# Kernel tuning notes

Hardware: AMD Instinct MI355X
Metric: run time of the kernel (lower is better)

## Reference

```python
import jax, jax.numpy as jnp
import numpy as np

D_MODEL = 1024
N_HEADS = 16
D_K = D_MODEL // N_HEADS  # 64
SCALE = 1.0 / np.sqrt(D_K).astype(np.float32)


def setup_inputs() -> dict:
    key = jax.random.key(0)
    kx, kq, kk, kv, ko = jax.random.split(key, 5)
    B, S = 2, 2048
    s = 0.02  # keep pre-softmax logits in a sane range
    return {
        "x": jax.random.normal(kx, (B, S, D_MODEL), dtype=jnp.float32),
        "Wq": jax.random.normal(kq, (D_MODEL, D_MODEL), dtype=jnp.float32) * s,
        "Wk": jax.random.normal(kk, (D_MODEL, D_MODEL), dtype=jnp.float32) * s,
        "Wv": jax.random.normal(kv, (D_MODEL, D_MODEL), dtype=jnp.float32) * s,
        "Wo": jax.random.normal(ko, (D_MODEL, D_MODEL), dtype=jnp.float32) * s,
    }


def reference(x, Wq, Wk, Wv, Wo):
    # x: [B, S, D]; nn.Linear(bias=False) computes x @ W.T
    B, S, D = x.shape
    H, dk = N_HEADS, D_K

    def proj(W):
        # [B, S, D] -> [B, H, S, dk]
        return (x @ W.T).reshape(B, S, H, dk).transpose(0, 2, 1, 3)

    q = proj(Wq)
    k = proj(Wk)
    v = proj(Wv)

    # Flash tiling with online softmax is exact full attention (no mask):
    scores = jnp.einsum("bhqd,bhkd->bhqk", q, k) * SCALE  # [B,H,S,S]
    p = jax.nn.softmax(scores, axis=-1)
    o = jnp.einsum("bhqk,bhkd->bhqd", p, v)               # [B,H,S,dk]

    o = o.transpose(0, 2, 1, 3).reshape(B, S, D)
    return o @ Wo.T
```

## Files before the change

kernel.cpp:

```cpp
#include <hip/hip_runtime.h>
#include <cstdint>

typedef __attribute__((ext_vector_type(8))) __bf16 bf16x8;
typedef __attribute__((ext_vector_type(4))) float f32x4;
using u16 = unsigned short;
using u32 = unsigned int;

#define D_MODEL 1024
#define N_HEADS 16
#define D_K     64
#define SEQ     2048
#define BATCH   2
#define NTOKENS (BATCH * SEQ)
#define SCALE   0.125f
#define LOG2E   1.44269504088896340736f
#define C2      (SCALE * LOG2E)

__device__ __forceinline__ u16 f32_to_bf16(float f) {
    union { float f; u32 u; } v; v.f = f;
    u32 r = (v.u + 0x7fffu + ((v.u >> 16) & 1u)) >> 16;
    return (u16)r;
}

__device__ __forceinline__ u32 cvt_pk_bf16(float a, float b) {
    u32 r;
    asm("v_cvt_pk_bf16_f32 %0, %1, %2" : "=v"(r) : "v"(a), "v"(b));
    return r;
}

typedef const __attribute__((address_space(1))) u32* gas_ptr;
typedef __attribute__((address_space(3))) u32* las_ptr;
__device__ __forceinline__ void gl2lds16(const u16* g, u16* l) {
    __builtin_amdgcn_global_load_lds((gas_ptr)g, (las_ptr)l, 16, 0, 0);
}

__global__ __launch_bounds__(256) void cvt_all(const float* __restrict__ x,
                                               const float* __restrict__ Wq, const float* __restrict__ Wk,
                                               const float* __restrict__ Wv, const float* __restrict__ Wo,
                                               u16* __restrict__ xb,
                                               u16* __restrict__ wq, u16* __restrict__ wk,
                                               u16* __restrict__ wv, u16* __restrict__ wo) {
    const int NX = NTOKENS * D_MODEL;
    size_t i = (size_t)(blockIdx.x * 256 + threadIdx.x) * 4;
    const float* src; u16* dst; size_t off;
    if (i < (size_t)NX) { src = x; dst = xb; off = i; }
    else {
        size_t j = i - NX;
        int w = (int)(j >> 20);
        off = j & ((1u << 20) - 1);
        src = (w == 0) ? Wq : (w == 1) ? Wk : (w == 2) ? Wv : Wo;
        dst = (w == 0) ? wq : (w == 1) ? wk : (w == 2) ? wv : wo;
    }
    float4 f = *(const float4*)(src + off);
    u32 lo = (u32)f32_to_bf16(f.x) | ((u32)f32_to_bf16(f.y) << 16);
    u32 hi = (u32)f32_to_bf16(f.z) | ((u32)f32_to_bf16(f.w) << 16);
    uint2 o; o.x = lo; o.y = hi;
    size_t osw = (off & ~(size_t)63) | ((((off >> 3) & 7) ^ ((off >> 10) & 7)) << 3) | (off & 7);
    *(uint2*)(dst + osw) = o;
}

__device__ __forceinline__ void gemm_core_128(const u16* __restrict__ Ab,
                                              const u16* __restrict__ Bb,
                                              u16* __restrict__ sm,
                                              f32x4 acc[4][4]) {
    const int tid  = threadIdx.x;
    const int wave = tid >> 6, lane = tid & 63;
    const int quad = lane >> 4, l4 = lane & 15, s7 = l4 & 7;
    const int wm = wave >> 1, wn = wave & 1;

    const int srow = tid >> 3, sch = tid & 7;
    const u16* Asrc = Ab + (size_t)srow * D_MODEL + sch * 8;
    const u16* Bsrc = Bb + (size_t)srow * D_MODEL + sch * 8;

#define STG8(base_, kt_) do {                                                         \
    const size_t ko_ = (size_t)(kt_) * 64;                                            \
    u16* const Ad_ = sm + (base_) + wave * 512;                                       \
    u16* const Bd_ = sm + (base_) + 8192 + wave * 512;                                \
    _Pragma("unroll")                                                                 \
    for (int c_ = 0; c_ < 4; c_++)                                                    \
        gl2lds16(Asrc + (size_t)c_ * 32 * D_MODEL + ko_, Ad_ + c_ * 2048);            \
    _Pragma("unroll")                                                                 \
    for (int c_ = 0; c_ < 4; c_++)                                                    \
        gl2lds16(Bsrc + (size_t)c_ * 32 * D_MODEL + ko_, Bd_ + c_ * 2048);            \
} while (0)

    STG8(0, 0);
    asm volatile("s_waitcnt vmcnt(0)" ::: "memory");
    __builtin_amdgcn_s_barrier();

    for (int kt = 0; kt < 16; ++kt) {
        const int cur = (kt & 1) << 14;
        if (kt < 15) {
            if (kt & 1) STG8(0, kt + 1); else STG8(16384, kt + 1);
        }
        const u16* Ar = sm + cur;
        const u16* Br = sm + cur + 8192;
        bf16x8 af[4][2], bfr[4][2];
#pragma unroll
        for (int mt = 0; mt < 4; mt++) {
            const int row = wm * 64 + mt * 16 + l4;
#pragma unroll
            for (int kk = 0; kk < 2; kk++)
                af[mt][kk] = *(const bf16x8*)&Ar[row * 64 + (((kk << 2) + quad) ^ s7) * 8];
        }
#pragma unroll
        for (int nt = 0; nt < 4; nt++) {
            const int row = wn * 64 + nt * 16 + l4;
#pragma unroll
            for (int kk = 0; kk < 2; kk++)
                bfr[nt][kk] = *(const bf16x8*)&Br[row * 64 + (((kk << 2) + quad) ^ s7) * 8];
        }
        __builtin_amdgcn_s_setprio(1);
#pragma unroll
        for (int kk = 0; kk < 2; kk++)
#pragma unroll
            for (int mt = 0; mt < 4; mt++)
#pragma unroll
                for (int nt = 0; nt < 4; nt++)
                    acc[mt][nt] = __builtin_amdgcn_mfma_f32_16x16x32_bf16(af[mt][kk], bfr[nt][kk], acc[mt][nt], 0, 0, 0);
        __builtin_amdgcn_s_setprio(0);
        asm volatile("s_waitcnt vmcnt(0)" ::: "memory");
        __builtin_amdgcn_s_barrier();
    }
#undef STG8
}

__global__ __launch_bounds__(256, 2) void gemm_qkv(const u16* __restrict__ xb,
                                                   const u16* __restrict__ wq,
                                                   const u16* __restrict__ wk,
                                                   const u16* __restrict__ wv,
                                                   u16* __restrict__ Qb, u16* __restrict__ Kb,
                                                   u16* __restrict__ Vt) {
    __shared__ __align__(16) u16 sm[32768];
    const int bid = blockIdx.x;
    const u16 *Ab, *Bb;
    int m0, n0, sel;
    if (bid < 512) {
        sel = bid >> 8;
        const int t = bid & 255;
        m0 = (t >> 3) * 128; n0 = (t & 7) * 128;
        Ab = xb + (size_t)m0 * D_MODEL;
        Bb = (sel ? wk : wq) + (size_t)n0 * D_MODEL;
    } else {
        sel = 2;
        const int t = bid - 512;
        m0 = (t >> 5) * 128; n0 = (t & 31) * 128;
        Ab = wv + (size_t)m0 * D_MODEL;
        Bb = xb + (size_t)n0 * D_MODEL;
    }

    f32x4 acc[4][4] = {};
    gemm_core_128(Ab, Bb, sm, acc);

    const int lane = threadIdx.x & 63, quad = lane >> 4, l4 = lane & 15;
    const int wave = threadIdx.x >> 6, wm = wave >> 1, wn = wave & 1;
#pragma unroll
    for (int mt = 0; mt < 4; mt++)
#pragma unroll
        for (int nt = 0; nt < 4; nt++)
#pragma unroll
            for (int r = 0; r < 4; r++) {
                const int mrow = wm * 64 + mt * 16 + quad * 4 + r;
                const int ncol = wn * 64 + nt * 16 + l4;
                const float v = acc[mt][nt][r];
                if (sel == 0)
                    Qb[(size_t)(m0 + mrow) * D_MODEL + n0 + ncol] = f32_to_bf16(v * C2);
                else if (sel == 1)
                    Kb[(size_t)(m0 + mrow) * D_MODEL + n0 + ncol] = f32_to_bf16(v);
                else
                    Vt[(size_t)(m0 + mrow) * NTOKENS + n0 + ncol] = f32_to_bf16(v);
            }
}

__global__ __launch_bounds__(256, 2) void gemm_out(const u16* __restrict__ A,
                                                   const u16* __restrict__ Bw,
                                                   float* __restrict__ C) {
    __shared__ __align__(16) u16 sm[32768];
    const int bid = blockIdx.x;
    const int m0 = (bid >> 3) * 128, n0 = (bid & 7) * 128;

    f32x4 acc[4][4] = {};
    gemm_core_128(A + (size_t)m0 * D_MODEL, Bw + (size_t)n0 * D_MODEL, sm, acc);

    const int lane = threadIdx.x & 63, quad = lane >> 4, l4 = lane & 15;
    const int wave = threadIdx.x >> 6, wm = wave >> 1, wn = wave & 1;
#pragma unroll
    for (int mt = 0; mt < 4; mt++)
#pragma unroll
        for (int nt = 0; nt < 4; nt++)
#pragma unroll
            for (int r = 0; r < 4; r++) {
                const int mrow = wm * 64 + mt * 16 + quad * 4 + r;
                const int ncol = wn * 64 + nt * 16 + l4;
                C[(size_t)(m0 + mrow) * D_MODEL + n0 + ncol] = acc[mt][nt][r];
            }
}

__global__ __launch_bounds__(512, 4) void attn(const u16* __restrict__ Q,
                                               const u16* __restrict__ K,
                                               const u16* __restrict__ Vt,
                                               u16* __restrict__ O) {
    __shared__ __align__(16) u16 smem[17664];
    u16* KsB = smem;
    u16* VsB = smem + 8192;
    const int KBUF = 4096, VBUF = 4096;

    const int tid  = threadIdx.x;
    const int wave = tid >> 6, lane = tid & 63;
    const int quad = lane >> 4, l4 = lane & 15;
    const int qg = wave & 3, kv = wave >> 2;
    const int bid = blockIdx.x;
    const int h  = (bid & 7) | (((bid >> 3) & 1) << 3);
    const int b  = (bid >> 4) & 1;
    const int q0 = (bid >> 5) * 128;
    const size_t headoff = (size_t)b * SEQ * D_MODEL + (size_t)h * D_K;

    const int sarr = tid >> 8;
    const int st   = tid & 255;
    const int srow = st >> 2, sc = st & 3;
    const int r7   = srow & 7;
    const u16* gsrc = (sarr == 0)
        ? K  + headoff + (size_t)srow * D_MODEL + sc * 16
        : Vt + (size_t)(h * 64 + srow) * NTOKENS + (size_t)b * SEQ + sc * 16;
    const size_t gstep = (sarr == 0) ? (size_t)64 * D_MODEL : 64;

    const int kd0 = srow * 64 + (((2 * sc)     ^ r7) * 8);
    const int kd1 = srow * 64 + (((2 * sc + 1) ^ r7) * 8);
    const int g32 = sc >> 1, vc = sc & 1;
    const int vw0 = srow * 64 + (((g32 * 4 + 0) ^ r7) * 8) + 4 * vc;
    const int vw1 = srow * 64 + (((g32 * 4 + 1) ^ r7) * 8) + 4 * vc;
    const int vw2 = srow * 64 + (((g32 * 4 + 2) ^ r7) * 8) + 4 * vc;
    const int vw3 = srow * 64 + (((g32 * 4 + 3) ^ r7) * 8) + 4 * vc;

    bf16x8 qa[2][2];
#pragma unroll
    for (int qs = 0; qs < 2; qs++) {
        const u16* qp = Q + headoff + (size_t)(q0 + qg * 32 + qs * 16 + l4) * D_MODEL + quad * 8;
        qa[qs][0] = *(const bf16x8*)qp;
        qa[qs][1] = *(const bf16x8*)(qp + 32);
    }

    union { u32 u[4]; bf16x8 v; } onesu;
#pragma unroll
    for (int i = 0; i < 4; i++) onesu.u[i] = 0x3F803F80u;

    int4 pr0 = *(const int4*)gsrc;
    int4 pr1 = *(const int4*)(gsrc + 8);

    f32x4 acc_o[2][4] = {};
    f32x4 acc_l[2] = {};

    const int sw7 = l4 & 7;

    for (int it = 0; it < 32; ++it) {
        if (sarr == 0) {
            u16* d = KsB + (it & 1) * KBUF;
            *(int4*)(d + kd0) = pr0;
            *(int4*)(d + kd1) = pr1;
        } else {
            u16* d = VsB + (it & 1) * VBUF;
            const uint2* h0 = (const uint2*)&pr0;
            const uint2* h1 = (const uint2*)&pr1;
            *(uint2*)(d + vw0) = h0[0];
            *(uint2*)(d + vw1) = h0[1];
            *(uint2*)(d + vw2) = h1[0];
            *(uint2*)(d + vw3) = h1[1];
        }
        __syncthreads();

        const u16* gn = gsrc + (size_t)((it + 1) & 31) * gstep;
        pr0 = *(const int4*)gn;
        pr1 = *(const int4*)(gn + 8);

        const u16* ksr = KsB + (it & 1) * KBUF;
        const u16* vsr = VsB + (it & 1) * VBUF;

        bf16x8 kb[2][2];
#pragma unroll
        for (int n2 = 0; n2 < 2; n2++) {
            const int krow = kv * 32 + n2 * 16 + l4;
            kb[n2][0] = *(const bf16x8*)&ksr[krow * 64 + ((quad       ^ sw7) * 8)];
            kb[n2][1] = *(const bf16x8*)&ksr[krow * 64 + (((4 + quad) ^ sw7) * 8)];
        }
        f32x4 sacc[2][2] = {};
        __builtin_amdgcn_s_setprio(1);
#pragma unroll
        for (int qs = 0; qs < 2; qs++)
#pragma unroll
            for (int n2 = 0; n2 < 2; n2++) {
                sacc[qs][n2] = __builtin_amdgcn_mfma_f32_16x16x32_bf16(kb[n2][0], qa[qs][0], sacc[qs][n2], 0, 0, 0);
                sacc[qs][n2] = __builtin_amdgcn_mfma_f32_16x16x32_bf16(kb[n2][1], qa[qs][1], sacc[qs][n2], 0, 0, 0);
            }
        __builtin_amdgcn_s_setprio(0);

        union { u32 u[4]; bf16x8 v; } pp[2];
#pragma unroll
        for (int qs = 0; qs < 2; qs++)
#pragma unroll
            for (int n2 = 0; n2 < 2; n2++) {
                float p0 = __builtin_amdgcn_exp2f(sacc[qs][n2][0]);
                float p1 = __builtin_amdgcn_exp2f(sacc[qs][n2][1]);
                float p2 = __builtin_amdgcn_exp2f(sacc[qs][n2][2]);
                float p3 = __builtin_amdgcn_exp2f(sacc[qs][n2][3]);
                pp[qs].u[n2 * 2]     = cvt_pk_bf16(p0, p1);
                pp[qs].u[n2 * 2 + 1] = cvt_pk_bf16(p2, p3);
            }

        __builtin_amdgcn_s_setprio(1);
#pragma unroll
        for (int dvt = 0; dvt < 4; dvt++) {
            const int vrow = dvt * 16 + l4;
            bf16x8 vfr = *(const bf16x8*)&vsr[vrow * 64 + ((((kv << 2) + quad) ^ sw7) * 8)];
#pragma unroll
            for (int qs = 0; qs < 2; qs++)
                acc_o[qs][dvt] = __builtin_amdgcn_mfma_f32_16x16x32_bf16(pp[qs].v, vfr, acc_o[qs][dvt], 0, 0, 0);
        }
#pragma unroll
        for (int qs = 0; qs < 2; qs++)
            acc_l[qs] = __builtin_amdgcn_mfma_f32_16x16x32_bf16(pp[qs].v, onesu.v, acc_l[qs], 0, 0, 0);
        __builtin_amdgcn_s_setprio(0);
    }

    const int OFS = 68;
    float* Of = (float*)smem;
    float* Lf = Of + 128 * OFS;
    __syncthreads();
    if (kv == 1) {
#pragma unroll
        for (int qs = 0; qs < 2; qs++) {
#pragma unroll
            for (int dvt = 0; dvt < 4; dvt++)
#pragma unroll
                for (int r = 0; r < 4; r++)
                    Of[(qg * 32 + qs * 16 + quad * 4 + r) * OFS + dvt * 16 + l4] = acc_o[qs][dvt][r];
            if (l4 == 0)
#pragma unroll
                for (int r = 0; r < 4; r++)
                    Lf[qg * 32 + qs * 16 + quad * 4 + r] = acc_l[qs][r];
        }
    }
    __syncthreads();
    if (kv == 0) {
#pragma unroll
        for (int qs = 0; qs < 2; qs++)
#pragma unroll
            for (int r = 0; r < 4; r++) {
                const int qi = qg * 32 + qs * 16 + quad * 4 + r;
                float ltot = acc_l[qs][r] + Lf[qi];
                float linv = 1.f / ltot;
                const int qrow = q0 + qi;
#pragma unroll
                for (int dvt = 0; dvt < 4; dvt++) {
                    float v = acc_o[qs][dvt][r] + Of[qi * OFS + dvt * 16 + l4];
                    const int csw = (((dvt * 2 + (l4 >> 3)) ^ (qrow & 7)) << 3) | (l4 & 7);
                    O[headoff + (size_t)qrow * D_MODEL + csw] = f32_to_bf16(v * linv);
                }
            }
    }
}

extern "C" void kernel_launch(void* const* d_in, const int* in_sizes, int n_in,
                              void* d_out, int out_size, void* d_ws, size_t ws_size,
                              hipStream_t stream) {
    const float* x  = (const float*)d_in[0];
    const float* Wq = (const float*)d_in[1];
    const float* Wk = (const float*)d_in[2];
    const float* Wv = (const float*)d_in[3];
    const float* Wo = (const float*)d_in[4];

    const int NW = D_MODEL * D_MODEL;

    char* ws = (char*)d_ws;
    u16* xb = (u16*)ws;
    u16* wq = (u16*)(ws + (8u << 20));
    u16* wk = wq + NW;
    u16* wv = wk + NW;
    u16* wo = wv + NW;
    u16* Qb  = (u16*)(ws + (16u << 20));
    u16* Kb  = (u16*)(ws + (24u << 20));
    u16* Vtb = (u16*)(ws + (32u << 20));

    cvt_all<<<8192, 256, 0, stream>>>(x, Wq, Wk, Wv, Wo, xb, wq, wk, wv, wo);

    gemm_qkv<<<768, 256, 0, stream>>>(xb, wq, wk, wv, Qb, Kb, Vtb);

    attn<<<512, 512, 0, stream>>>(Qb, Kb, Vtb, xb);

    gemm_out<<<256, 256, 0, stream>>>(xb, wo, (float*)d_out);
}
```

Before: 178.9 us.

## Halve attention block size to 64 queries with 4 waves, doubling grid

The attention kernel now uses 256-thread blocks covering 64 query rows instead of 512 threads and 128 rows, and launches 1024 blocks instead of 512. Each thread now stages both K and V tiles rather than splitting the loads between the two thread halves. The aim is more blocks across the CUs and lighter barriers. The cost is that each K/V tile is fetched from global memory by twice as many blocks, and each thread holds more prefetch registers.

```diff
diff --git a/kernel.cpp b/kernel.cpp
--- a/kernel.cpp
+++ b/kernel.cpp
@@ -196,11 +196,11 @@
             }
 }
 
-__global__ __launch_bounds__(512, 4) void attn(const u16* __restrict__ Q,
+__global__ __launch_bounds__(256, 4) void attn(const u16* __restrict__ Q,
                                                const u16* __restrict__ K,
                                                const u16* __restrict__ Vt,
                                                u16* __restrict__ O) {
-    __shared__ __align__(16) u16 smem[17664];
+    __shared__ __align__(16) u16 smem[16384];
     u16* KsB = smem;
     u16* VsB = smem + 8192;
     const int KBUF = 4096, VBUF = 4096;
@@ -208,21 +208,17 @@
     const int tid  = threadIdx.x;
     const int wave = tid >> 6, lane = tid & 63;
     const int quad = lane >> 4, l4 = lane & 15;
-    const int qg = wave & 3, kv = wave >> 2;
+    const int qg = wave & 1, kv = wave >> 1;
     const int bid = blockIdx.x;
     const int h  = (bid & 7) | (((bid >> 3) & 1) << 3);
     const int b  = (bid >> 4) & 1;
-    const int q0 = (bid >> 5) * 128;
+    const int q0 = (bid >> 5) * 64;
     const size_t headoff = (size_t)b * SEQ * D_MODEL + (size_t)h * D_K;
 
-    const int sarr = tid >> 8;
-    const int st   = tid & 255;
-    const int srow = st >> 2, sc = st & 3;
+    const int srow = tid >> 2, sc = tid & 3;
     const int r7   = srow & 7;
-    const u16* gsrc = (sarr == 0)
-        ? K  + headoff + (size_t)srow * D_MODEL + sc * 16
-        : Vt + (size_t)(h * 64 + srow) * NTOKENS + (size_t)b * SEQ + sc * 16;
-    const size_t gstep = (sarr == 0) ? (size_t)64 * D_MODEL : 64;
+    const u16* gK = K  + headoff + (size_t)srow * D_MODEL + sc * 16;
+    const u16* gV = Vt + (size_t)(h * 64 + srow) * NTOKENS + (size_t)b * SEQ + sc * 16;
 
     const int kd0 = srow * 64 + (((2 * sc)     ^ r7) * 8);
     const int kd1 = srow * 64 + (((2 * sc + 1) ^ r7) * 8);
@@ -244,8 +240,10 @@
 #pragma unroll
     for (int i = 0; i < 4; i++) onesu.u[i] = 0x3F803F80u;
 
-    int4 pr0 = *(const int4*)gsrc;
-    int4 pr1 = *(const int4*)(gsrc + 8);
+    int4 pk0 = *(const int4*)gK;
+    int4 pk1 = *(const int4*)(gK + 8);
+    int4 pv0 = *(const int4*)gV;
+    int4 pv1 = *(const int4*)(gV + 8);
 
     f32x4 acc_o[2][4] = {};
     f32x4 acc_l[2] = {};
@@ -253,24 +251,27 @@
     const int sw7 = l4 & 7;
 
     for (int it = 0; it < 32; ++it) {
-        if (sarr == 0) {
+        {
             u16* d = KsB + (it & 1) * KBUF;
-            *(int4*)(d + kd0) = pr0;
-            *(int4*)(d + kd1) = pr1;
-        } else {
-            u16* d = VsB + (it & 1) * VBUF;
-            const uint2* h0 = (const uint2*)&pr0;
-            const uint2* h1 = (const uint2*)&pr1;
-            *(uint2*)(d + vw0) = h0[0];
-            *(uint2*)(d + vw1) = h0[1];
-            *(uint2*)(d + vw2) = h1[0];
-            *(uint2*)(d + vw3) = h1[1];
+            *(int4*)(d + kd0) = pk0;
+            *(int4*)(d + kd1) = pk1;
+            u16* dv = VsB + (it & 1) * VBUF;
+            const uint2* h0 = (const uint2*)&pv0;
+            const uint2* h1 = (const uint2*)&pv1;
+            *(uint2*)(dv + vw0) = h0[0];
+            *(uint2*)(dv + vw1) = h0[1];
+            *(uint2*)(dv + vw2) = h1[0];
+            *(uint2*)(dv + vw3) = h1[1];
         }
         __syncthreads();
 
-        const u16* gn = gsrc + (size_t)((it + 1) & 31) * gstep;
-        pr0 = *(const int4*)gn;
-        pr1 = *(const int4*)(gn + 8);
+        const int nx = (it + 1) & 31;
+        const u16* gkn = gK + (size_t)nx * 64 * D_MODEL;
+        const u16* gvn = gV + (size_t)nx * 64;
+        pk0 = *(const int4*)gkn;
+        pk1 = *(const int4*)(gkn + 8);
+        pv0 = *(const int4*)gvn;
+        pv1 = *(const int4*)(gvn + 8);
 
         const u16* ksr = KsB + (it & 1) * KBUF;
         const u16* vsr = VsB + (it & 1) * VBUF;
@@ -323,7 +324,7 @@
 
     const int OFS = 68;
     float* Of = (float*)smem;
-    float* Lf = Of + 128 * OFS;
+    float* Lf = Of + 64 * OFS;
     __syncthreads();
     if (kv == 1) {
 #pragma unroll
@@ -384,7 +385,7 @@
 
     gemm_qkv<<<768, 256, 0, stream>>>(xb, wq, wk, wv, Qb, Kb, Vtb);
 
-    attn<<<512, 512, 0, stream>>>(Qb, Kb, Vtb, xb);
+    attn<<<1024, 256, 0, stream>>>(Qb, Kb, Vtb, xb);
 
     gemm_out<<<256, 256, 0, stream>>>(xb, wo, (float*)d_out);
 }
```

After: 181.3 us. Within noise of the previous version (+1.3%).

## Use direct global-to-LDS loads in attention with pre-swizzled K/V layout

Applied to the files above, without the earlier changes.

The QKV GEMM epilogue now writes K and Vt in the swizzled order the attention kernel expects in LDS. This lets attention copy tiles with gl2lds16 direct global-to-LDS loads instead of staging through registers and scattering. The attention block shrinks from 512 to 256 threads, so each wave covers all 64 keys per tile rather than splitting keys across two wave groups. That removes the cross-wave LDS reduction of O and l at the end, at the cost of more MFMA work per wave and fewer waves per block to hide latency.

```diff
diff --git a/kernel.cpp b/kernel.cpp
--- a/kernel.cpp
+++ b/kernel.cpp
@@ -163,12 +163,19 @@
                 const int mrow = wm * 64 + mt * 16 + quad * 4 + r;
                 const int ncol = wn * 64 + nt * 16 + l4;
                 const float v = acc[mt][nt][r];
-                if (sel == 0)
+                const int m7 = (quad * 4 + r) & 7;
+                if (sel == 0) {
                     Qb[(size_t)(m0 + mrow) * D_MODEL + n0 + ncol] = f32_to_bf16(v * C2);
-                else if (sel == 1)
-                    Kb[(size_t)(m0 + mrow) * D_MODEL + n0 + ncol] = f32_to_bf16(v);
-                else
-                    Vt[(size_t)(m0 + mrow) * NTOKENS + n0 + ncol] = f32_to_bf16(v);
+                } else if (sel == 1) {
+                    const int csw = (wn * 64) | ((((nt * 2 + (l4 >> 3)) ^ m7) << 3)) | (l4 & 7);
+                    Kb[(size_t)(m0 + mrow) * D_MODEL + n0 + csw] = f32_to_bf16(v);
+                } else {
+                    const int k  = nt * 16 + l4;
+                    const int g  = (k >> 2) & 3, c = (k >> 4) & 1, r_ = k & 3;
+                    const int s  = (k & 32) | (g * 8 + c * 4 + r_);
+                    const int csw = (wn * 64) | ((((s >> 3) ^ m7) << 3)) | (s & 7);
+                    Vt[(size_t)(m0 + mrow) * NTOKENS + n0 + csw] = f32_to_bf16(v);
+                }
             }
 }
 
@@ -196,41 +203,40 @@
             }
 }
 
-__global__ __launch_bounds__(512, 4) void attn(const u16* __restrict__ Q,
+__global__ __launch_bounds__(256, 4) void attn(const u16* __restrict__ Q,
                                                const u16* __restrict__ K,
                                                const u16* __restrict__ Vt,
                                                u16* __restrict__ O) {
-    __shared__ __align__(16) u16 smem[17664];
+    __shared__ __align__(16) u16 smem[16384];
     u16* KsB = smem;
     u16* VsB = smem + 8192;
-    const int KBUF = 4096, VBUF = 4096;
 
     const int tid  = threadIdx.x;
     const int wave = tid >> 6, lane = tid & 63;
     const int quad = lane >> 4, l4 = lane & 15;
-    const int qg = wave & 3, kv = wave >> 2;
+    const int qg = wave;
     const int bid = blockIdx.x;
     const int h  = (bid & 7) | (((bid >> 3) & 1) << 3);
     const int b  = (bid >> 4) & 1;
     const int q0 = (bid >> 5) * 128;
     const size_t headoff = (size_t)b * SEQ * D_MODEL + (size_t)h * D_K;
 
-    const int sarr = tid >> 8;
-    const int st   = tid & 255;
-    const int srow = st >> 2, sc = st & 3;
-    const int r7   = srow & 7;
-    const u16* gsrc = (sarr == 0)
-        ? K  + headoff + (size_t)srow * D_MODEL + sc * 16
-        : Vt + (size_t)(h * 64 + srow) * NTOKENS + (size_t)b * SEQ + sc * 16;
-    const size_t gstep = (sarr == 0) ? (size_t)64 * D_MODEL : 64;
-
-    const int kd0 = srow * 64 + (((2 * sc)     ^ r7) * 8);
-    const int kd1 = srow * 64 + (((2 * sc + 1) ^ r7) * 8);
-    const int g32 = sc >> 1, vc = sc & 1;
-    const int vw0 = srow * 64 + (((g32 * 4 + 0) ^ r7) * 8) + 4 * vc;
-    const int vw1 = srow * 64 + (((g32 * 4 + 1) ^ r7) * 8) + 4 * vc;
-    const int vw2 = srow * 64 + (((g32 * 4 + 2) ^ r7) * 8) + 4 * vc;
-    const int vw3 = srow * 64 + (((g32 * 4 + 3) ^ r7) * 8) + 4 * vc;
+    const int srow8 = lane >> 3, sch = lane & 7;
+    const u16* srcK = K  + headoff + (size_t)(wave * 16 + srow8) * D_MODEL + sch * 8;
+    const u16* srcV = Vt + (size_t)(h * 64 + wave * 16 + srow8) * NTOKENS + (size_t)b * SEQ + sch * 8;
+    u16* const dK0 = KsB + (wave * 16) * 64;
+    u16* const dK1 = KsB + (wave * 16 + 8) * 64;
+    u16* const dV0 = VsB + (wave * 16) * 64;
+    u16* const dV1 = VsB + (wave * 16 + 8) * 64;
+
+#define ASTG(buf_, t_) do {                                                  \
+    const size_t kt_ = (size_t)(t_) * 64 * D_MODEL;                          \
+    const size_t vt_ = (size_t)(t_) * 64;                                    \
+    gl2lds16(srcK + kt_,                       dK0 + (buf_));                \
+    gl2lds16(srcK + kt_ + 8 * D_MODEL,         dK1 + (buf_));                \
+    gl2lds16(srcV + vt_,                       dV0 + (buf_));                \
+    gl2lds16(srcV + vt_ + (size_t)8 * NTOKENS, dV1 + (buf_));                \
+} while (0)
 
     bf16x8 qa[2][2];
 #pragma unroll
@@ -244,119 +250,89 @@
 #pragma unroll
     for (int i = 0; i < 4; i++) onesu.u[i] = 0x3F803F80u;
 
-    int4 pr0 = *(const int4*)gsrc;
-    int4 pr1 = *(const int4*)(gsrc + 8);
-
     f32x4 acc_o[2][4] = {};
     f32x4 acc_l[2] = {};
-
     const int sw7 = l4 & 7;
 
+    ASTG(0, 0);
+    asm volatile("s_waitcnt vmcnt(0)" ::: "memory");
+    __builtin_amdgcn_s_barrier();
+
     for (int it = 0; it < 32; ++it) {
-        if (sarr == 0) {
-            u16* d = KsB + (it & 1) * KBUF;
-            *(int4*)(d + kd0) = pr0;
-            *(int4*)(d + kd1) = pr1;
-        } else {
-            u16* d = VsB + (it & 1) * VBUF;
-            const uint2* h0 = (const uint2*)&pr0;
-            const uint2* h1 = (const uint2*)&pr1;
-            *(uint2*)(d + vw0) = h0[0];
-            *(uint2*)(d + vw1) = h0[1];
-            *(uint2*)(d + vw2) = h1[0];
-            *(uint2*)(d + vw3) = h1[1];
-        }
-        __syncthreads();
-
-        const u16* gn = gsrc + (size_t)((it + 1) & 31) * gstep;
-        pr0 = *(const int4*)gn;
-        pr1 = *(const int4*)(gn + 8);
-
-        const u16* ksr = KsB + (it & 1) * KBUF;
-        const u16* vsr = VsB + (it & 1) * VBUF;
-
-        bf16x8 kb[2][2];
-#pragma unroll
-        for (int n2 = 0; n2 < 2; n2++) {
-            const int krow = kv * 32 + n2 * 16 + l4;
-            kb[n2][0] = *(const bf16x8*)&ksr[krow * 64 + ((quad       ^ sw7) * 8)];
-            kb[n2][1] = *(const bf16x8*)&ksr[krow * 64 + (((4 + quad) ^ sw7) * 8)];
-        }
-        f32x4 sacc[2][2] = {};
-        __builtin_amdgcn_s_setprio(1);
-#pragma unroll
-        for (int qs = 0; qs < 2; qs++)
-#pragma unroll
-            for (int n2 = 0; n2 < 2; n2++) {
-                sacc[qs][n2] = __builtin_amdgcn_mfma_f32_16x16x32_bf16(kb[n2][0], qa[qs][0], sacc[qs][n2], 0, 0, 0);
-                sacc[qs][n2] = __builtin_amdgcn_mfma_f32_16x16x32_bf16(kb[n2][1], qa[qs][1], sacc[qs][n2], 0, 0, 0);
-            }
-        __builtin_amdgcn_s_setprio(0);
-
-        union { u32 u[4]; bf16x8 v; } pp[2];
-#pragma unroll
-        for (int qs = 0; qs < 2; qs++)
-#pragma unroll
-            for (int n2 = 0; n2 < 2; n2++) {
-                float p0 = __builtin_amdgcn_exp2f(sacc[qs][n2][0]);
-                float p1 = __builtin_amdgcn_exp2f(sacc[qs][n2][1]);
-                float p2 = __builtin_amdgcn_exp2f(sacc[qs][n2][2]);
-                float p3 = __builtin_amdgcn_exp2f(sacc[qs][n2][3]);
-                pp[qs].u[n2 * 2]     = cvt_pk_bf16(p0, p1);
-                pp[qs].u[n2 * 2 + 1] = cvt_pk_bf16(p2, p3);
-            }
+        const int cur = (it & 1) ? 4096 : 0;
+        if (it < 31) { if (it & 1) ASTG(0, it + 1); else ASTG(4096, it + 1); }
+        const u16* ksr = KsB + cur;
+        const u16* vsr = VsB + cur;
+
+        union { u32 u[4]; bf16x8 v; } pp[2][2];
+#pragma unroll
+        for (int kf = 0; kf < 2; kf++) {
+            bf16x8 kb[2][2];
+#pragma unroll
+            for (int n2p = 0; n2p < 2; n2p++) {
+                const int krow = kf * 32 + n2p * 16 + l4;
+                kb[n2p][0] = *(const bf16x8*)&ksr[krow * 64 + ((quad       ^ sw7) * 8)];
+                kb[n2p][1] = *(const bf16x8*)&ksr[krow * 64 + (((4 + quad) ^ sw7) * 8)];
+            }
+            f32x4 sacc[2][2] = {};
+            __builtin_amdgcn_s_setprio(1);
+#pragma unroll
+            for (int qs = 0; qs < 2; qs++)
+#pragma unroll
+                for (int n2p = 0; n2p < 2; n2p++) {
+                    sacc[qs][n2p] = __builtin_amdgcn_mfma_f32_16x16x32_bf16(kb[n2p][0], qa[qs][0], sacc[qs][n2p], 0, 0, 0);
+                    sacc[qs][n2p] = __builtin_amdgcn_mfma_f32_16x16x32_bf16(kb[n2p][1], qa[qs][1], sacc[qs][n2p], 0, 0, 0);
+                }
+            __builtin_amdgcn_s_setprio(0);
+#pragma unroll
+            for (int qs = 0; qs < 2; qs++)
+#pragma unroll
+                for (int n2p = 0; n2p < 2; n2p++) {
+                    float p0 = __builtin_amdgcn_exp2f(sacc[qs][n2p][0]);
+                    float p1 = __builtin_amdgcn_exp2f(sacc[qs][n2p][1]);
+                    float p2 = __builtin_amdgcn_exp2f(sacc[qs][n2p][2]);
+                    float p3 = __builtin_amdgcn_exp2f(sacc[qs][n2p][3]);
+                    pp[qs][kf].u[n2p * 2]     = cvt_pk_bf16(p0, p1);
+                    pp[qs][kf].u[n2p * 2 + 1] = cvt_pk_bf16(p2, p3);
+                }
+        }
 
         __builtin_amdgcn_s_setprio(1);
 #pragma unroll
         for (int dvt = 0; dvt < 4; dvt++) {
             const int vrow = dvt * 16 + l4;
-            bf16x8 vfr = *(const bf16x8*)&vsr[vrow * 64 + ((((kv << 2) + quad) ^ sw7) * 8)];
-#pragma unroll
-            for (int qs = 0; qs < 2; qs++)
-                acc_o[qs][dvt] = __builtin_amdgcn_mfma_f32_16x16x32_bf16(pp[qs].v, vfr, acc_o[qs][dvt], 0, 0, 0);
+#pragma unroll
+            for (int kf = 0; kf < 2; kf++) {
+                bf16x8 vfr = *(const bf16x8*)&vsr[vrow * 64 + ((((kf << 2) + quad) ^ sw7) * 8)];
+#pragma unroll
+                for (int qs = 0; qs < 2; qs++)
+                    acc_o[qs][dvt] = __builtin_amdgcn_mfma_f32_16x16x32_bf16(pp[qs][kf].v, vfr, acc_o[qs][dvt], 0, 0, 0);
+            }
         }
 #pragma unroll
         for (int qs = 0; qs < 2; qs++)
-            acc_l[qs] = __builtin_amdgcn_mfma_f32_16x16x32_bf16(pp[qs].v, onesu.v, acc_l[qs], 0, 0, 0);
+#pragma unroll
+            for (int kf = 0; kf < 2; kf++)
+                acc_l[qs] = __builtin_amdgcn_mfma_f32_16x16x32_bf16(pp[qs][kf].v, onesu.v, acc_l[qs], 0, 0, 0);
         __builtin_amdgcn_s_setprio(0);
-    }
-
-    const int OFS = 68;
-    float* Of = (float*)smem;
-    float* Lf = Of + 128 * OFS;
-    __syncthreads();
-    if (kv == 1) {
-#pragma unroll
-        for (int qs = 0; qs < 2; qs++) {
-#pragma unroll
-            for (int dvt = 0; dvt < 4; dvt++)
-#pragma unroll
-                for (int r = 0; r < 4; r++)
-                    Of[(qg * 32 + qs * 16 + quad * 4 + r) * OFS + dvt * 16 + l4] = acc_o[qs][dvt][r];
-            if (l4 == 0)
-#pragma unroll
-                for (int r = 0; r < 4; r++)
-                    Lf[qg * 32 + qs * 16 + quad * 4 + r] = acc_l[qs][r];
-        }
-    }
-    __syncthreads();
-    if (kv == 0) {
-#pragma unroll
-        for (int qs = 0; qs < 2; qs++)
-#pragma unroll
-            for (int r = 0; r < 4; r++) {
-                const int qi = qg * 32 + qs * 16 + quad * 4 + r;
-                float ltot = acc_l[qs][r] + Lf[qi];
-                float linv = 1.f / ltot;
-                const int qrow = q0 + qi;
-#pragma unroll
-                for (int dvt = 0; dvt < 4; dvt++) {
-                    float v = acc_o[qs][dvt][r] + Of[qi * OFS + dvt * 16 + l4];
-                    const int csw = (((dvt * 2 + (l4 >> 3)) ^ (qrow & 7)) << 3) | (l4 & 7);
-                    O[headoff + (size_t)qrow * D_MODEL + csw] = f32_to_bf16(v * linv);
-                }
-            }
-    }
+
+        asm volatile("s_waitcnt vmcnt(0)" ::: "memory");
+        __builtin_amdgcn_s_barrier();
+    }
+
+#pragma unroll
+    for (int qs = 0; qs < 2; qs++)
+#pragma unroll
+        for (int r = 0; r < 4; r++) {
+            const float linv = 1.f / acc_l[qs][r];
+            const int qrow = q0 + qg * 32 + qs * 16 + quad * 4 + r;
+#pragma unroll
+            for (int dvt = 0; dvt < 4; dvt++) {
+                const int csw = (((dvt * 2 + (l4 >> 3)) ^ (qrow & 7)) << 3) | (l4 & 7);
+                O[headoff + (size_t)qrow * D_MODEL + csw] = f32_to_bf16(acc_o[qs][dvt][r] * linv);
+            }
+        }
+#undef ASTG
 }
 
 extern "C" void kernel_launch(void* const* d_in, const int* in_sizes, int n_in,
@@ -384,7 +360,7 @@
 
     gemm_qkv<<<768, 256, 0, stream>>>(xb, wq, wk, wv, Qb, Kb, Vtb);
 
-    attn<<<512, 512, 0, stream>>>(Qb, Kb, Vtb, xb);
+    attn<<<512, 256, 0, stream>>>(Qb, Kb, Vtb, xb);
 
     gemm_out<<<256, 256, 0, stream>>>(xb, wo, (float*)d_out);
 }
```

New measurement: 181.5 us. Within noise of the previous version (+1.5%).
